# Performance work log

Measured on AMD Instinct MI355X. Metric: run time of the kernel, lower is better.

Reference implementation:

```python
import jax, jax.numpy as jnp
import numpy as np

N_HEADS = 16
ROPE_THETA = 10000.0


def _rope(x):
    # x: (b, h, t, d). Interleaved-pair rotary embedding (lucidrains
    # rotary_embedding_torch convention: rotate_half on (d r) pairs, r=2).
    b, h, t, d = x.shape
    inv_freq = 1.0 / (ROPE_THETA ** (jnp.arange(0, d, 2, dtype=jnp.float32) / d))  # (d/2,)
    ang = jnp.arange(t, dtype=jnp.float32)[:, None] * inv_freq[None, :]            # (t, d/2)
    cos = jnp.cos(ang)
    sin = jnp.sin(ang)
    xp = x.reshape(b, h, t, d // 2, 2)
    x1, x2 = xp[..., 0], xp[..., 1]
    o1 = x1 * cos - x2 * sin
    o2 = x1 * sin + x2 * cos
    return jnp.stack([o1, o2], axis=-1).reshape(b, h, t, d)


def setup_inputs() -> dict:
    key = jax.random.key(0)
    k1, k2, k3 = jax.random.split(key, 3)
    B, T, C = 4, 2048, 1024
    x = jax.random.normal(k1, (B, T, C), dtype=jnp.float32)
    # torch nn.Linear weight layout: (out_features, in_features)
    w_attn = jax.random.normal(k2, (3 * C, C), dtype=jnp.float32) * (1.0 / np.sqrt(C))
    w_proj = jax.random.normal(k3, (C, C), dtype=jnp.float32) * (1.0 / np.sqrt(C))
    return {"x": x, "w_attn": w_attn, "w_proj": w_proj}


def reference(x, w_attn, w_proj):
    B, T, C = x.shape
    H = N_HEADS
    D = C // H
    # fused QKV projection: (b, t, 3C)
    qkv = jnp.einsum('btc,fc->btf', x, w_attn)
    # rearrange 'b t (r h d) -> r b h t d'
    qkv = qkv.reshape(B, T, 3, H, D).transpose(2, 0, 3, 1, 4)
    q, k, v = qkv[0], qkv[1], qkv[2]
    q = _rope(q)
    k = _rope(k)
    scale = 1.0 / np.sqrt(D).astype(np.float32)
    scores = jnp.einsum('bhqd,bhkd->bhqk', q, k) * scale
    attn = jax.nn.softmax(scores, axis=-1)
    y = jnp.einsum('bhqk,bhkd->bhqd', attn, v)       # (b, h, t, d)
    y = y.transpose(0, 2, 1, 3).reshape(B, T, C)     # 'b h t d -> b t (h d)'
    return jnp.einsum('btc,oc->bto', y, w_proj)
```

## Files before the change

kernel.cpp:

```cpp
#include <hip/hip_runtime.h>
#include <hip/hip_bf16.h>
#include <math.h>

typedef __bf16 bf16;
typedef float f32x4 __attribute__((ext_vector_type(4)));
typedef bf16 bf16x8 __attribute__((ext_vector_type(8)));
typedef bf16 bf16x4 __attribute__((ext_vector_type(4)));
typedef unsigned int uint;

#define MFMA16(a, b, c) __builtin_amdgcn_mfma_f32_16x16x32_bf16(a, b, c, 0, 0, 0)

static constexpr int T_SEQ = 2048;
static constexpr int CDIM  = 1024;
static constexpr int NH    = 16;
static constexpr int DH    = 64;
static constexpr float FREQ_C = 0.20762050593045998f;

__device__ __forceinline__ void gld_lds16(const bf16* g, bf16* l) {
    __builtin_amdgcn_global_load_lds(
        (const __attribute__((address_space(1))) void*)g,
        (__attribute__((address_space(3))) void*)l, 16, 0, 0);
}

__device__ __forceinline__ uint pack_bf16(float a, float b) {
    union { bf16 h; unsigned short u; } ca, cb;
    ca.h = (bf16)a; cb.h = (bf16)b;
    return (uint)ca.u | ((uint)cb.u << 16);
}

__device__ __forceinline__ void fast_sincos(float x, float* s, float* c) {
    const float INV2PI = 0.15915494309189535f;
    const float PI2_HI = 6.28125f;
    const float PI2_LO = 1.9353071795864769e-3f;
    const float n = rintf(x * INV2PI);
    float r = fmaf(-n, PI2_HI, x);
    r = fmaf(-n, PI2_LO, r);
    *s = __sinf(r);
    *c = __cosf(r);
}

__global__ __launch_bounds__(256)
void cvt_f32_bf16(const float* __restrict__ in, bf16* __restrict__ out, int n8) {
    const int i = blockIdx.x * 256 + threadIdx.x;
    if (i >= n8) return;
    const f32x4* p = (const f32x4*)(in + (size_t)i * 8);
    const f32x4 lo = p[0], hi = p[1];
    bf16x8 o;
    o[0] = (bf16)lo[0]; o[1] = (bf16)lo[1]; o[2] = (bf16)lo[2]; o[3] = (bf16)lo[3];
    o[4] = (bf16)hi[0]; o[5] = (bf16)hi[1]; o[6] = (bf16)hi[2]; o[7] = (bf16)hi[3];
    *(bf16x8*)(out + (size_t)i * 8) = o;
}

#define GEMM_CORE(Abase, Bbase, KDIM)                                            \
    f32x4 acc[4][4] = {};                                                        \
    for (int kk = 0; kk < (KDIM); kk += 64) {                                    \
        __syncthreads();                                                         \
        _Pragma("unroll")                                                        \
        for (int u = 0; u < 4; u++) {                                            \
            const int st = wave * 4 + u, mg = st >> 1, kg = st & 1;              \
            gld_lds16(Abase + (size_t)(mg * 16 + sm) * (KDIM) + kk + kg * 32 + sc * 8, \
                      &ash[st * 512]);                                           \
            gld_lds16(Bbase + (size_t)(mg * 16 + sm) * (KDIM) + kk + kg * 32 + sc * 8, \
                      &bsh[st * 512]);                                           \
        }                                                                        \
        __syncthreads();                                                         \
        _Pragma("unroll")                                                        \
        for (int kg = 0; kg < 2; kg++) {                                         \
            bf16x8 af[4], bfr[4];                                                \
            _Pragma("unroll")                                                    \
            for (int a = 0; a < 4; a++)                                          \
                af[a] = *(const bf16x8*)&ash[((wm * 4 + a) * 2 + kg) * 512 + lane * 8]; \
            _Pragma("unroll")                                                    \
            for (int b = 0; b < 4; b++)                                          \
                bfr[b] = *(const bf16x8*)&bsh[((wn * 4 + b) * 2 + kg) * 512 + lane * 8]; \
            _Pragma("unroll")                                                    \
            for (int a = 0; a < 4; a++)                                          \
                _Pragma("unroll")                                                \
                for (int b = 0; b < 4; b++)                                      \
                    acc[a][b] = MFMA16(af[a], bfr[b], acc[a][b]);                \
        }                                                                        \
    }

__global__ __launch_bounds__(256)
void gemm_qkv(const bf16* __restrict__ X, const bf16* __restrict__ W,
              bf16* __restrict__ Qo, bf16* __restrict__ Ko, bf16* __restrict__ Vt) {
    __shared__ __align__(16) bf16 ash[16 * 512];
    __shared__ __align__(16) bf16 bsh[16 * 512];
    const int tid = threadIdx.x, lane = tid & 63, wave = tid >> 6;
    const int quad = lane >> 4, l16 = lane & 15;
    const int wm = wave >> 1, wn = wave & 1;
    const int bm = blockIdx.y, bn = blockIdx.x;
    const int sm = lane & 15, sc = lane >> 4;

    const bf16* Abase = X + (size_t)(bm * 128) * CDIM;
    const bf16* Bbase = W + (size_t)(bn * 128) * CDIM;
    GEMM_CORE(Abase, Bbase, CDIM)

    const int rr    = (bn * 128) >> 10;
    const int nsec  = (bn * 128) & 1023;
    const int batch = (bm * 128) >> 11;
    const int tb    = ((bm * 128) & 2047) + wm * 64;

    if (rr == 2) {
#pragma unroll
        for (int b = 0; b < 4; b++) {
            const int n = nsec + wn * 64 + b * 16 + l16;
            const int h = n >> 6, d = n & 63;
            bf16* vp = Vt + ((size_t)(batch * NH + h) * DH + d) * T_SEQ;
#pragma unroll
            for (int a = 0; a < 4; a++) {
                const int t0 = tb + a * 16 + quad * 4;
                bf16x4 pk4 = { (bf16)acc[a][b][0], (bf16)acc[a][b][1],
                               (bf16)acc[a][b][2], (bf16)acc[a][b][3] };
                *(bf16x4*)(vp + t0) = pk4;
            }
        }
    } else {
        bf16* Dst = (rr == 0) ? Qo : Ko;
        const float scale = (rr == 0) ? 0.125f : 1.0f;
#pragma unroll
        for (int b = 0; b < 4; b++) {
            const int n = nsec + wn * 64 + b * 16 + l16;
            const int h = n >> 6, d = n & 63;
            const float invf = exp2f(-(float)(d & ~1) * FREQ_C);
            const int odd = d & 1;
            bf16* dp = Dst + (size_t)(batch * NH + h) * T_SEQ * DH + d;
#pragma unroll
            for (int a = 0; a < 4; a++) {
#pragma unroll
                for (int r = 0; r < 4; r++) {
                    const int t = tb + a * 16 + quad * 4 + r;
                    const float val = acc[a][b][r];
                    const float partner = __shfl_xor(val, 1);
                    float sn, cs;
                    fast_sincos((float)t * invf, &sn, &cs);
                    float o = odd ? (partner * sn + val * cs)
                                  : (val * cs - partner * sn);
                    dp[(size_t)t * DH] = (bf16)(o * scale);
                }
            }
        }
    }
}

__global__ __launch_bounds__(256)
void gemm_proj(const bf16* __restrict__ X, const bf16* __restrict__ W,
               float* __restrict__ Out) {
    __shared__ __align__(16) bf16 ash[16 * 512];
    __shared__ __align__(16) bf16 bsh[16 * 512];
    const int tid = threadIdx.x, lane = tid & 63, wave = tid >> 6;
    const int quad = lane >> 4, l16 = lane & 15;
    const int wm = wave >> 1, wn = wave & 1;
    const int bm = blockIdx.y, bn = blockIdx.x;
    const int sm = lane & 15, sc = lane >> 4;

    const bf16* Abase = X + (size_t)(bm * 128) * CDIM;
    const bf16* Bbase = W + (size_t)(bn * 128) * CDIM;
    GEMM_CORE(Abase, Bbase, CDIM)

#pragma unroll
    for (int b = 0; b < 4; b++) {
        const int n = bn * 128 + wn * 64 + b * 16 + l16;
#pragma unroll
        for (int a = 0; a < 4; a++) {
            const int m = bm * 128 + wm * 64 + a * 16 + quad * 4;
#pragma unroll
            for (int r = 0; r < 4; r++)
                Out[(size_t)(m + r) * CDIM + n] = acc[a][b][r];
        }
    }
}

__global__ __launch_bounds__(256)
void flash(const bf16* __restrict__ Q, const bf16* __restrict__ K,
           const bf16* __restrict__ Vt, bf16* __restrict__ Y) {
    __shared__ __align__(16) bf16 ksh[8 * 512];
    __shared__ __align__(16) bf16 vsh[8 * 512];
    const int tid = threadIdx.x, lane = tid & 63, wave = tid >> 6;
    const int quad = lane >> 4, l16 = lane & 15;
    const int id = blockIdx.x;
    const int bh = (id & 7) * 8 + ((id >> 3) & 7);
    const int qb = id >> 6;
    const size_t kbase = (size_t)bh * T_SEQ * DH;
    const size_t vbase = (size_t)bh * DH * T_SEQ;
    const int q0 = qb * 128 + wave * 32;

    bf16x8 bq[2][2];
#pragma unroll
    for (int g = 0; g < 2; g++) {
        const bf16* qp = Q + kbase + (size_t)(q0 + g * 16 + l16) * DH + quad * 8;
        bq[g][0] = *(const bf16x8*)qp;
        bq[g][1] = *(const bf16x8*)(qp + 32);
    }

    f32x4 oT[2][4] = {};
    float li[2] = {0.f, 0.f};

    const int perm0 = (((quad & 1) * 2) * 16 + l16) * 4;
    const int perm1 = perm0 + 64;
    const int kgsel = quad >> 1;

    for (int kt = 0; kt < T_SEQ; kt += 64) {
        __syncthreads();
        if (wave < 2) {
#pragma unroll
            for (int u = 0; u < 4; u++) {
                const int s = wave * 4 + u, kg = s >> 1, kh = s & 1;
                gld_lds16(K + kbase + (size_t)(kt + kg * 16 + l16) * DH
                              + kh * 32 + quad * 8,
                          &ksh[s * 512]);
            }
        } else {
#pragma unroll
            for (int u = 0; u < 4; u++) {
                const int s = (wave - 2) * 4 + u, dg = s >> 1, kh = s & 1;
                gld_lds16(Vt + vbase + (size_t)(dg * 16 + l16) * T_SEQ
                              + kt + kh * 32 + quad * 8,
                          &vsh[s * 512]);
            }
        }
        __syncthreads();

        uint pk[2][4][2];
        {
            bf16x8 kf[4][2];
#pragma unroll
            for (int kg = 0; kg < 4; kg++) {
                kf[kg][0] = *(const bf16x8*)&ksh[(kg * 2 + 0) * 512 + lane * 8];
                kf[kg][1] = *(const bf16x8*)&ksh[(kg * 2 + 1) * 512 + lane * 8];
            }
#pragma unroll
            for (int g = 0; g < 2; g++) {
                f32x4 s4[4] = {};
#pragma unroll
                for (int kg = 0; kg < 4; kg++) {
                    s4[kg] = MFMA16(kf[kg][0], bq[g][0], s4[kg]);
                    s4[kg] = MFMA16(kf[kg][1], bq[g][1], s4[kg]);
                }
#pragma unroll
                for (int kg = 0; kg < 4; kg++) {
                    const float e0 = __expf(s4[kg][0]), e1 = __expf(s4[kg][1]);
                    const float e2 = __expf(s4[kg][2]), e3 = __expf(s4[kg][3]);
                    li[g] += (e0 + e1) + (e2 + e3);
                    pk[g][kg][0] = pack_bf16(e0, e1);
                    pk[g][kg][1] = pack_bf16(e2, e3);
                }
            }
        }

#pragma unroll
        for (int kh = 0; kh < 2; kh++) {
            bf16x8 va[4];
#pragma unroll
            for (int dg = 0; dg < 4; dg++)
                va[dg] = *(const bf16x8*)&vsh[(dg * 2 + kh) * 512 + lane * 8];
#pragma unroll
            for (int g = 0; g < 2; g++) {
                const uint dA0 = pk[g][kh * 2][0],     dA1 = pk[g][kh * 2][1];
                const uint dB0 = pk[g][kh * 2 + 1][0], dB1 = pk[g][kh * 2 + 1][1];
                const uint a0 = (uint)__builtin_amdgcn_ds_bpermute(perm0, (int)dA0);
                const uint b0 = (uint)__builtin_amdgcn_ds_bpermute(perm0, (int)dB0);
                const uint a1 = (uint)__builtin_amdgcn_ds_bpermute(perm0, (int)dA1);
                const uint b1 = (uint)__builtin_amdgcn_ds_bpermute(perm0, (int)dB1);
                const uint a2 = (uint)__builtin_amdgcn_ds_bpermute(perm1, (int)dA0);
                const uint b2 = (uint)__builtin_amdgcn_ds_bpermute(perm1, (int)dB0);
                const uint a3 = (uint)__builtin_amdgcn_ds_bpermute(perm1, (int)dA1);
                const uint b3 = (uint)__builtin_amdgcn_ds_bpermute(perm1, (int)dB1);
                union { uint u[4]; bf16x8 v; } bP;
                bP.u[0] = kgsel ? b0 : a0;
                bP.u[1] = kgsel ? b1 : a1;
                bP.u[2] = kgsel ? b2 : a2;
                bP.u[3] = kgsel ? b3 : a3;
#pragma unroll
                for (int dg = 0; dg < 4; dg++)
                    oT[g][dg] = MFMA16(va[dg], bP.v, oT[g][dg]);
            }
        }
    }

    const int b = bh >> 4, h = bh & 15;
#pragma unroll
    for (int g = 0; g < 2; g++) {
        float lg = li[g];
        lg += __shfl_xor(lg, 16);
        lg += __shfl_xor(lg, 32);
        const float inv = 1.0f / lg;
        const size_t yrow = ((size_t)b * T_SEQ + q0 + g * 16 + l16) * CDIM + h * DH;
#pragma unroll
        for (int dg = 0; dg < 4; dg++)
#pragma unroll
            for (int r = 0; r < 4; r++)
                Y[yrow + dg * 16 + quad * 4 + r] = (bf16)(oT[g][dg][r] * inv);
    }
}

extern "C" void kernel_launch(void* const* d_in, const int* in_sizes, int n_in,
                              void* d_out, int out_size, void* d_ws, size_t ws_size,
                              hipStream_t stream) {
    const float* x      = (const float*)d_in[0];
    const float* w_attn = (const float*)d_in[1];
    const float* w_proj = (const float*)d_in[2];
    float* out = (float*)d_out;

    bf16* ws = (bf16*)d_ws;
    const size_t SZ = (size_t)4 * NH * T_SEQ * DH;
    bf16* Xb  = ws;
    bf16* Wab = Xb + SZ;
    bf16* Wpb = Wab + 3145728;
    bf16* Qb  = Wpb + 1048576;
    bf16* Kb  = Qb + SZ;
    bf16* Vtb = Kb + SZ;
    bf16* Yb  = Vtb + SZ;

    cvt_f32_bf16<<<4096, 256, 0, stream>>>(x, Xb, 1048576);
    cvt_f32_bf16<<<1536, 256, 0, stream>>>(w_attn, Wab, 393216);
    cvt_f32_bf16<<<512, 256, 0, stream>>>(w_proj, Wpb, 131072);

    gemm_qkv<<<dim3(24, 64), 256, 0, stream>>>(Xb, Wab, Qb, Kb, Vtb);
    flash<<<1024, 256, 0, stream>>>(Qb, Kb, Vtb, Yb);
    gemm_proj<<<dim3(8, 64), 256, 0, stream>>>(Yb, Wpb, out);
}
```

Measured before the change: 367.7 us.

## Switch flash attention to 32x32 MFMA and precompute RoPE sin/cos table

The flash kernel now uses 32x32x16 bf16 MFMA tiles. This changes the K/V LDS staging layout, and the P-matrix redistribution becomes a single xor-32 shuffle in place of the ds_bpermute chains. A separate kernel precomputes a cos/sin table for RoPE, which the QKV GEMM epilogue reads instead of evaluating sincos per element. The aim is fewer instructions and less permute traffic in the attention inner loop, plus less transcendental work in the epilogue. The cost is an extra kernel launch, extra table reads, and higher register pressure from the 16-wide accumulators.

After: 360.9 us. About the same (-1.9%).

```diff
diff --git a/kernel.cpp b/kernel.cpp
--- a/kernel.cpp
+++ b/kernel.cpp
@@ -4,11 +4,13 @@
 
 typedef __bf16 bf16;
 typedef float f32x4 __attribute__((ext_vector_type(4)));
+typedef float f32x16 __attribute__((ext_vector_type(16)));
 typedef bf16 bf16x8 __attribute__((ext_vector_type(8)));
 typedef bf16 bf16x4 __attribute__((ext_vector_type(4)));
 typedef unsigned int uint;
 
 #define MFMA16(a, b, c) __builtin_amdgcn_mfma_f32_16x16x32_bf16(a, b, c, 0, 0, 0)
+#define MFMA32(a, b, c) __builtin_amdgcn_mfma_f32_32x32x16_bf16(a, b, c, 0, 0, 0)
 
 static constexpr int T_SEQ = 2048;
 static constexpr int CDIM  = 1024;
@@ -20,12 +22,6 @@
     __builtin_amdgcn_global_load_lds(
         (const __attribute__((address_space(1))) void*)g,
         (__attribute__((address_space(3))) void*)l, 16, 0, 0);
-}
-
-__device__ __forceinline__ uint pack_bf16(float a, float b) {
-    union { bf16 h; unsigned short u; } ca, cb;
-    ca.h = (bf16)a; cb.h = (bf16)b;
-    return (uint)ca.u | ((uint)cb.u << 16);
 }
 
 __device__ __forceinline__ void fast_sincos(float x, float* s, float* c) {
@@ -37,6 +33,16 @@
     r = fmaf(-n, PI2_LO, r);
     *s = __sinf(r);
     *c = __cosf(r);
+}
+
+__global__ __launch_bounds__(256)
+void rope_table(float2* __restrict__ tab) {
+    const int i = blockIdx.x * 256 + threadIdx.x;
+    const int t = i >> 5, p = i & 31;
+    const float ang = (float)t * exp2f(-2.0f * (float)p * FREQ_C);
+    float s, c;
+    fast_sincos(ang, &s, &c);
+    tab[i] = make_float2(c, s);
 }
 
 __global__ __launch_bounds__(256)
@@ -83,7 +89,8 @@
 
 __global__ __launch_bounds__(256)
 void gemm_qkv(const bf16* __restrict__ X, const bf16* __restrict__ W,
-              bf16* __restrict__ Qo, bf16* __restrict__ Ko, bf16* __restrict__ Vt) {
+              bf16* __restrict__ Qo, bf16* __restrict__ Ko, bf16* __restrict__ Vt,
+              const float2* __restrict__ tab) {
     __shared__ __align__(16) bf16 ash[16 * 512];
     __shared__ __align__(16) bf16 bsh[16 * 512];
     const int tid = threadIdx.x, lane = tid & 63, wave = tid >> 6;
@@ -122,8 +129,7 @@
         for (int b = 0; b < 4; b++) {
             const int n = nsec + wn * 64 + b * 16 + l16;
             const int h = n >> 6, d = n & 63;
-            const float invf = exp2f(-(float)(d & ~1) * FREQ_C);
-            const int odd = d & 1;
+            const int p = d >> 1, odd = d & 1;
             bf16* dp = Dst + (size_t)(batch * NH + h) * T_SEQ * DH + d;
 #pragma unroll
             for (int a = 0; a < 4; a++) {
@@ -132,10 +138,9 @@
                     const int t = tb + a * 16 + quad * 4 + r;
                     const float val = acc[a][b][r];
                     const float partner = __shfl_xor(val, 1);
-                    float sn, cs;
-                    fast_sincos((float)t * invf, &sn, &cs);
-                    float o = odd ? (partner * sn + val * cs)
-                                  : (val * cs - partner * sn);
+                    const float2 cs = tab[t * 32 + p];
+                    float o = odd ? (partner * cs.y + val * cs.x)
+                                  : (val * cs.x - partner * cs.y);
                     dp[(size_t)t * DH] = (bf16)(o * scale);
                 }
             }
@@ -177,7 +182,7 @@
     __shared__ __align__(16) bf16 ksh[8 * 512];
     __shared__ __align__(16) bf16 vsh[8 * 512];
     const int tid = threadIdx.x, lane = tid & 63, wave = tid >> 6;
-    const int quad = lane >> 4, l16 = lane & 15;
+    const int l32 = lane & 31, hi = lane >> 5;
     const int id = blockIdx.x;
     const int bh = (id & 7) * 8 + ((id >> 3) & 7);
     const int qb = id >> 6;
@@ -185,113 +190,88 @@
     const size_t vbase = (size_t)bh * DH * T_SEQ;
     const int q0 = qb * 128 + wave * 32;
 
-    bf16x8 bq[2][2];
-#pragma unroll
-    for (int g = 0; g < 2; g++) {
-        const bf16* qp = Q + kbase + (size_t)(q0 + g * 16 + l16) * DH + quad * 8;
-        bq[g][0] = *(const bf16x8*)qp;
-        bq[g][1] = *(const bf16x8*)(qp + 32);
-    }
-
-    f32x4 oT[2][4] = {};
-    float li[2] = {0.f, 0.f};
-
-    const int perm0 = (((quad & 1) * 2) * 16 + l16) * 4;
-    const int perm1 = perm0 + 64;
-    const int kgsel = quad >> 1;
+    bf16x8 bq[4];
+    const bf16* qp = Q + kbase + (size_t)(q0 + l32) * DH + hi * 8;
+#pragma unroll
+    for (int c = 0; c < 4; c++) bq[c] = *(const bf16x8*)(qp + c * 16);
+
+    f32x16 oT[2] = {};
+    float li = 0.f;
 
     for (int kt = 0; kt < T_SEQ; kt += 64) {
         __syncthreads();
         if (wave < 2) {
 #pragma unroll
             for (int u = 0; u < 4; u++) {
-                const int s = wave * 4 + u, kg = s >> 1, kh = s & 1;
-                gld_lds16(K + kbase + (size_t)(kt + kg * 16 + l16) * DH
-                              + kh * 32 + quad * 8,
+                const int s = wave * 4 + u, kb = s >> 2, c = s & 3;
+                gld_lds16(K + kbase + (size_t)(kt + kb * 32 + l32) * DH
+                              + c * 16 + hi * 8,
                           &ksh[s * 512]);
             }
         } else {
 #pragma unroll
             for (int u = 0; u < 4; u++) {
-                const int s = (wave - 2) * 4 + u, dg = s >> 1, kh = s & 1;
-                gld_lds16(Vt + vbase + (size_t)(dg * 16 + l16) * T_SEQ
-                              + kt + kh * 32 + quad * 8,
+                const int s = (wave - 2) * 4 + u, db = s >> 2, kc = s & 3;
+                gld_lds16(Vt + vbase + (size_t)(db * 32 + l32) * T_SEQ
+                              + kt + kc * 16 + hi * 8,
                           &vsh[s * 512]);
             }
         }
         __syncthreads();
 
-        uint pk[2][4][2];
-        {
-            bf16x8 kf[4][2];
-#pragma unroll
-            for (int kg = 0; kg < 4; kg++) {
-                kf[kg][0] = *(const bf16x8*)&ksh[(kg * 2 + 0) * 512 + lane * 8];
-                kf[kg][1] = *(const bf16x8*)&ksh[(kg * 2 + 1) * 512 + lane * 8];
-            }
-#pragma unroll
-            for (int g = 0; g < 2; g++) {
-                f32x4 s4[4] = {};
-#pragma unroll
-                for (int kg = 0; kg < 4; kg++) {
-                    s4[kg] = MFMA16(kf[kg][0], bq[g][0], s4[kg]);
-                    s4[kg] = MFMA16(kf[kg][1], bq[g][1], s4[kg]);
+#pragma unroll
+        for (int kb = 0; kb < 2; kb++) {
+            f32x16 s = {};
+#pragma unroll
+            for (int c = 0; c < 4; c++) {
+                const bf16x8 a = *(const bf16x8*)&ksh[(kb * 4 + c) * 512 + lane * 8];
+                s = MFMA32(a, bq[c], s);
+            }
+            uint P[8], S8[8];
+#pragma unroll
+            for (int w = 0; w < 8; w++) {
+                const float e0 = __expf(s[2 * w]);
+                const float e1 = __expf(s[2 * w + 1]);
+                li += e0 + e1;
+                union { __hip_bfloat162 v; uint u; } cv;
+                cv.v = __float22bfloat162_rn(make_float2(e0, e1));
+                P[w] = cv.u;
+            }
+#pragma unroll
+            for (int w = 0; w < 8; w++)
+                S8[w] = (uint)__shfl_xor((int)P[w], 32);
+#pragma unroll
+            for (int t = 0; t < 2; t++) {
+                union { uint u[4]; bf16x8 v; } bP;
+                bP.u[0] = hi ? S8[4 * t + 2] : P[4 * t + 0];
+                bP.u[1] = hi ? S8[4 * t + 3] : P[4 * t + 1];
+                bP.u[2] = hi ? P[4 * t + 2] : S8[4 * t + 0];
+                bP.u[3] = hi ? P[4 * t + 3] : S8[4 * t + 1];
+                const int kc = kb * 2 + t;
+#pragma unroll
+                for (int db = 0; db < 2; db++) {
+                    const bf16x8 a = *(const bf16x8*)&vsh[(db * 4 + kc) * 512 + lane * 8];
+                    oT[db] = MFMA32(a, bP.v, oT[db]);
                 }
-#pragma unroll
-                for (int kg = 0; kg < 4; kg++) {
-                    const float e0 = __expf(s4[kg][0]), e1 = __expf(s4[kg][1]);
-                    const float e2 = __expf(s4[kg][2]), e3 = __expf(s4[kg][3]);
-                    li[g] += (e0 + e1) + (e2 + e3);
-                    pk[g][kg][0] = pack_bf16(e0, e1);
-                    pk[g][kg][1] = pack_bf16(e2, e3);
-                }
-            }
-        }
-
-#pragma unroll
-        for (int kh = 0; kh < 2; kh++) {
-            bf16x8 va[4];
-#pragma unroll
-            for (int dg = 0; dg < 4; dg++)
-                va[dg] = *(const bf16x8*)&vsh[(dg * 2 + kh) * 512 + lane * 8];
-#pragma unroll
-            for (int g = 0; g < 2; g++) {
-                const uint dA0 = pk[g][kh * 2][0],     dA1 = pk[g][kh * 2][1];
-                const uint dB0 = pk[g][kh * 2 + 1][0], dB1 = pk[g][kh * 2 + 1][1];
-                const uint a0 = (uint)__builtin_amdgcn_ds_bpermute(perm0, (int)dA0);
-                const uint b0 = (uint)__builtin_amdgcn_ds_bpermute(perm0, (int)dB0);
-                const uint a1 = (uint)__builtin_amdgcn_ds_bpermute(perm0, (int)dA1);
-                const uint b1 = (uint)__builtin_amdgcn_ds_bpermute(perm0, (int)dB1);
-                const uint a2 = (uint)__builtin_amdgcn_ds_bpermute(perm1, (int)dA0);
-                const uint b2 = (uint)__builtin_amdgcn_ds_bpermute(perm1, (int)dB0);
-                const uint a3 = (uint)__builtin_amdgcn_ds_bpermute(perm1, (int)dA1);
-                const uint b3 = (uint)__builtin_amdgcn_ds_bpermute(perm1, (int)dB1);
-                union { uint u[4]; bf16x8 v; } bP;
-                bP.u[0] = kgsel ? b0 : a0;
-                bP.u[1] = kgsel ? b1 : a1;
-                bP.u[2] = kgsel ? b2 : a2;
-                bP.u[3] = kgsel ? b3 : a3;
-#pragma unroll
-                for (int dg = 0; dg < 4; dg++)
-                    oT[g][dg] = MFMA16(va[dg], bP.v, oT[g][dg]);
             }
         }
     }
 
+    li += __shfl_xor(li, 32);
+    const float inv = 1.0f / li;
+
     const int b = bh >> 4, h = bh & 15;
-#pragma unroll
-    for (int g = 0; g < 2; g++) {
-        float lg = li[g];
-        lg += __shfl_xor(lg, 16);
-        lg += __shfl_xor(lg, 32);
-        const float inv = 1.0f / lg;
-        const size_t yrow = ((size_t)b * T_SEQ + q0 + g * 16 + l16) * CDIM + h * DH;
-#pragma unroll
-        for (int dg = 0; dg < 4; dg++)
-#pragma unroll
-            for (int r = 0; r < 4; r++)
-                Y[yrow + dg * 16 + quad * 4 + r] = (bf16)(oT[g][dg][r] * inv);
-    }
+    const size_t yrow = ((size_t)b * T_SEQ + q0 + l32) * CDIM + h * DH;
+#pragma unroll
+    for (int db = 0; db < 2; db++)
+#pragma unroll
+        for (int rg = 0; rg < 4; rg++) {
+            bf16x4 o4 = { (bf16)(oT[db][rg * 4 + 0] * inv),
+                          (bf16)(oT[db][rg * 4 + 1] * inv),
+                          (bf16)(oT[db][rg * 4 + 2] * inv),
+                          (bf16)(oT[db][rg * 4 + 3] * inv) };
+            *(bf16x4*)(Y + yrow + db * 32 + 8 * rg + 4 * hi) = o4;
+        }
 }
 
 extern "C" void kernel_launch(void* const* d_in, const int* in_sizes, int n_in,
@@ -311,12 +291,14 @@
     bf16* Kb  = Qb + SZ;
     bf16* Vtb = Kb + SZ;
     bf16* Yb  = Vtb + SZ;
-
+    float2* tab = (float2*)(Yb + SZ);
+
+    rope_table<<<256, 256, 0, stream>>>(tab);
     cvt_f32_bf16<<<4096, 256, 0, stream>>>(x, Xb, 1048576);
     cvt_f32_bf16<<<1536, 256, 0, stream>>>(w_attn, Wab, 393216);
     cvt_f32_bf16<<<512, 256, 0, stream>>>(w_proj, Wpb, 131072);
 
-    gemm_qkv<<<dim3(24, 64), 256, 0, stream>>>(Xb, Wab, Qb, Kb, Vtb);
+    gemm_qkv<<<dim3(24, 64), 256, 0, stream>>>(Xb, Wab, Qb, Kb, Vtb, tab);
     flash<<<1024, 256, 0, stream>>>(Qb, Kb, Vtb, Yb);
     gemm_proj<<<dim3(8, 64), 256, 0, stream>>>(Yb, Wpb, out);
 }
```
